# Performance work log

Measured on AMD Instinct MI355X. Metric: run time of the kernel, lower is better.

Reference implementation:

```python
import jax, jax.numpy as jnp
import numpy as np

N_EMBED = 768
N_HEAD = 12
HEAD = N_EMBED // N_HEAD
B, T = 4, 2048


def setup_inputs() -> dict:
    key = jax.random.key(0)
    ks = jax.random.split(key, 12)
    s = 0.02
    d = N_EMBED
    return {
        "x": jax.random.normal(ks[0], (B, T, d), jnp.float32),
        "ln1_g": jnp.ones((d,), jnp.float32),
        "ln1_b": jnp.zeros((d,), jnp.float32),
        "w_attn": jax.random.normal(ks[1], (d, 3 * d), jnp.float32) * s,
        "b_attn": jnp.zeros((3 * d,), jnp.float32),
        "w_aproj": jax.random.normal(ks[2], (d, d), jnp.float32) * s,
        "b_aproj": jnp.zeros((d,), jnp.float32),
        "ln2_g": jnp.ones((d,), jnp.float32),
        "ln2_b": jnp.zeros((d,), jnp.float32),
        "w_fc": jax.random.normal(ks[3], (d, 4 * d), jnp.float32) * s,
        "b_fc": jnp.zeros((4 * d,), jnp.float32),
        "w_mproj": jax.random.normal(ks[4], (4 * d, d), jnp.float32) * s,
        "b_mproj": jnp.zeros((d,), jnp.float32),
    }


def _layernorm(x, g, b, eps=1e-5):
    mu = jnp.mean(x, axis=-1, keepdims=True)
    var = jnp.var(x, axis=-1, keepdims=True)
    return (x - mu) * jax.lax.rsqrt(var + eps) * g + b


def _attn(x, w_attn, b_attn, w_aproj, b_aproj):
    Bq, Tq, C = x.shape
    qkv = x @ w_attn + b_attn  # [B,T,3C]
    q, k, v = jnp.split(qkv, 3, axis=2)
    q = q.reshape(Bq, Tq, N_HEAD, HEAD).transpose(0, 2, 1, 3)  # [B,H,T,hd]
    k = k.reshape(Bq, Tq, N_HEAD, HEAD).transpose(0, 2, 1, 3)
    v = v.reshape(Bq, Tq, N_HEAD, HEAD).transpose(0, 2, 1, 3)
    att = jnp.einsum("bhqd,bhkd->bhqk", q, k) * (1.0 / np.sqrt(HEAD))
    causal = jnp.tril(jnp.ones((Tq, Tq), bool))
    att = jnp.where(causal, att, -jnp.inf)
    att = jax.nn.softmax(att, axis=-1)
    y = jnp.einsum("bhqk,bhkd->bhqd", att, v)
    y = y.transpose(0, 2, 1, 3).reshape(Bq, Tq, C)
    return y @ w_aproj + b_aproj


def reference(x, ln1_g, ln1_b, w_attn, b_attn, w_aproj, b_aproj,
              ln2_g, ln2_b, w_fc, b_fc, w_mproj, b_mproj):
    x = x + _attn(_layernorm(x, ln1_g, ln1_b), w_attn, b_attn, w_aproj, b_aproj)
    h = _layernorm(x, ln2_g, ln2_b)
    h = jax.nn.gelu(h @ w_fc + b_fc, approximate=False)
    x = x + (h @ w_mproj + b_mproj)
    return x
```

## Files before the change

### kernel.cpp

```cpp
#include <hip/hip_runtime.h>
#include <hip/hip_bf16.h>

#define NE 768
#define NH 12
#define HD 64
#define BB 4
#define TT 2048
#define ROWS (BB*TT)

typedef __attribute__((ext_vector_type(8))) short bf16x8;
typedef __attribute__((ext_vector_type(4))) float f32x4;

__device__ __forceinline__ short f2bf(float f) {
  __hip_bfloat16 h = __float2bfloat16(f);
  union { __hip_bfloat16 h; short s; } u; u.h = h; return u.s;
}

__device__ __forceinline__ void gload16(const void* g, void* l) {
  __builtin_amdgcn_global_load_lds(
      (const __attribute__((address_space(1))) void*)g,
      (__attribute__((address_space(3))) void*)l,
      16, 0, 0);
}

__device__ __forceinline__ void xcd_remap(int id, int nbn, int& bm, int& bn) {
  int x = id & 7;
  int j = id >> 3;
  bm = x * 8 + j / nbn;
  bn = j % nbn;
}

__global__ __launch_bounds__(256) void wtrans_kernel(
    const float* __restrict__ W, short* __restrict__ Wt, int K, int N) {
  __shared__ short tile[64 * 65];
  int k0 = blockIdx.x * 64, n0 = blockIdx.y * 64;
  int t = threadIdx.x;
#pragma unroll
  for (int p = 0; p < 16; ++p) {
    int idx = p * 256 + t;
    int r = idx >> 6, c = idx & 63;
    tile[r * 65 + c] = f2bf(W[(size_t)(k0 + r) * N + n0 + c]);
  }
  __syncthreads();
#pragma unroll
  for (int p = 0; p < 16; ++p) {
    int idx = p * 256 + t;
    int rr = idx >> 6, cc = idx & 63;
    Wt[(size_t)(n0 + rr) * K + k0 + cc] = tile[cc * 65 + rr];
  }
}

__global__ __launch_bounds__(256) void vtrans_kernel(
    const short* __restrict__ qkv, short* __restrict__ vt) {
  __shared__ short tile[64 * 65];
  int bh = blockIdx.x;
  int b = bh / NH, h = bh % NH;
  int t0 = blockIdx.y * 64;
  int t = threadIdx.x;
#pragma unroll
  for (int p = 0; p < 16; ++p) {
    int idx = p * 256 + t;
    int r = idx >> 6, c = idx & 63;
    tile[r * 65 + c] =
        qkv[(size_t)(b * TT + t0 + r) * (3 * NE) + 2 * NE + h * HD + c];
  }
  __syncthreads();
#pragma unroll
  for (int p = 0; p < 16; ++p) {
    int idx = p * 256 + t;
    int rr = idx >> 6, cc = idx & 63;
    vt[(size_t)bh * HD * TT + (size_t)rr * TT + t0 + cc] = tile[cc * 65 + rr];
  }
}

__global__ __launch_bounds__(64) void ln_kernel(
    const float* __restrict__ x, const float* __restrict__ g,
    const float* __restrict__ b, short* __restrict__ out) {
  int row = blockIdx.x, l = threadIdx.x;
  const float* xr = x + (size_t)row * NE;
  float4 v[3];
  float s = 0.f, ss = 0.f;
#pragma unroll
  for (int i = 0; i < 3; ++i) {
    v[i] = *reinterpret_cast<const float4*>(xr + l * 4 + i * 256);
    s += v[i].x + v[i].y + v[i].z + v[i].w;
    ss += v[i].x * v[i].x + v[i].y * v[i].y + v[i].z * v[i].z + v[i].w * v[i].w;
  }
#pragma unroll
  for (int m = 1; m < 64; m <<= 1) {
    s += __shfl_xor(s, m);
    ss += __shfl_xor(ss, m);
  }
  float mu = s * (1.0f / NE);
  float var = ss * (1.0f / NE) - mu * mu;
  float rstd = rsqrtf(var + 1e-5f);
#pragma unroll
  for (int i = 0; i < 3; ++i) {
    float4 gv = *reinterpret_cast<const float4*>(g + l * 4 + i * 256);
    float4 bv = *reinterpret_cast<const float4*>(b + l * 4 + i * 256);
    short4 o;
    o.x = f2bf((v[i].x - mu) * rstd * gv.x + bv.x);
    o.y = f2bf((v[i].y - mu) * rstd * gv.y + bv.y);
    o.z = f2bf((v[i].z - mu) * rstd * gv.z + bv.z);
    o.w = f2bf((v[i].w - mu) * rstd * gv.w + bv.w);
    *reinterpret_cast<short4*>(out + (size_t)row * NE + l * 4 + i * 256) = o;
  }
}

template <int EPI>
__global__ __launch_bounds__(256) void gemm_kernel(
    const short* __restrict__ A, const short* __restrict__ Bt,
    const float* __restrict__ bias, const float* __restrict__ resid,
    void* __restrict__ Cout, int M, int N, int K, int nbn) {
  __shared__ short As[2][128 * 32];
  __shared__ short Bs[2][128 * 32];
  int t = threadIdx.x;
  int w = t >> 6, l = t & 63;
  int wr = w >> 1, wc = w & 1;
  int bm, bn;
  xcd_remap(blockIdx.x, nbn, bm, bn);
  int lr = l & 15, g4 = l >> 4;

  f32x4 acc[4][4];
#pragma unroll
  for (int i = 0; i < 4; ++i)
#pragma unroll
    for (int j = 0; j < 4; ++j) acc[i][j] = (f32x4){0.f, 0.f, 0.f, 0.f};

  int r0 = t >> 2;
  int cs = ((t & 3) ^ (r0 & 3)) * 8;
  const short* ga = A + (size_t)(bm * 128) * K;
  const short* gb = Bt + (size_t)(bn * 128) * K;

  gload16(ga + (size_t)r0 * K + cs, &As[0][t * 8]);
  gload16(ga + (size_t)(r0 + 64) * K + cs, &As[0][(t + 256) * 8]);
  gload16(gb + (size_t)r0 * K + cs, &Bs[0][t * 8]);
  gload16(gb + (size_t)(r0 + 64) * K + cs, &Bs[0][(t + 256) * 8]);

  int xorA = (lr & 3) << 4;
  int nk = K >> 5;
  for (int kt = 0; kt < nk; ++kt) {
    int bi = kt & 1;
    __syncthreads();
    if (kt + 1 < nk) {
      int ko = (kt + 1) * 32;
      gload16(ga + (size_t)r0 * K + ko + cs, &As[bi ^ 1][t * 8]);
      gload16(ga + (size_t)(r0 + 64) * K + ko + cs, &As[bi ^ 1][(t + 256) * 8]);
      gload16(gb + (size_t)r0 * K + ko + cs, &Bs[bi ^ 1][t * 8]);
      gload16(gb + (size_t)(r0 + 64) * K + ko + cs, &Bs[bi ^ 1][(t + 256) * 8]);
    }
    const char* Ab = (const char*)As[bi];
    const char* Bb = (const char*)Bs[bi];
    bf16x8 af[4], bfr[4];
#pragma unroll
    for (int i = 0; i < 4; ++i)
      af[i] = *reinterpret_cast<const bf16x8*>(
          Ab + (((wr * 64 + i * 16 + lr) * 64 + g4 * 16) ^ xorA));
#pragma unroll
    for (int j = 0; j < 4; ++j)
      bfr[j] = *reinterpret_cast<const bf16x8*>(
          Bb + (((wc * 64 + j * 16 + lr) * 64 + g4 * 16) ^ xorA));
#pragma unroll
    for (int i = 0; i < 4; ++i)
#pragma unroll
      for (int j = 0; j < 4; ++j)
        acc[i][j] = __builtin_amdgcn_mfma_f32_16x16x32_bf16(af[i], bfr[j], acc[i][j], 0, 0, 0);
  }

  int rbase = bm * 128 + wr * 64;
  int cbase = bn * 128 + wc * 64;
#pragma unroll
  for (int i = 0; i < 4; ++i) {
#pragma unroll
    for (int r = 0; r < 4; ++r) {
      int row = rbase + i * 16 + g4 * 4 + r;
#pragma unroll
      for (int j = 0; j < 4; ++j) {
        int col = cbase + j * 16 + lr;
        float v = acc[i][j][r] + bias[col];
        if (EPI == 0) {
          ((short*)Cout)[(size_t)row * N + col] = f2bf(v);
        } else if (EPI == 1) {
          v = 0.5f * v * (1.0f + erff(v * 0.70710678118654752f));
          ((short*)Cout)[(size_t)row * N + col] = f2bf(v);
        } else {
          ((float*)Cout)[(size_t)row * N + col] = v + resid[(size_t)row * N + col];
        }
      }
    }
  }
}

template <int EPI>
__global__ __launch_bounds__(256) void gemm64_kernel(
    const short* __restrict__ A, const short* __restrict__ Bt,
    const float* __restrict__ bias, const float* __restrict__ resid,
    void* __restrict__ Cout, int M, int N, int K, int nbn) {
  __shared__ short As[2][128 * 32];
  __shared__ short Bs[2][64 * 32];
  int t = threadIdx.x;
  int w = t >> 6, l = t & 63;
  int bm, bn;
  xcd_remap(blockIdx.x, nbn, bm, bn);
  int lr = l & 15, g4 = l >> 4;

  f32x4 acc[2][4];
#pragma unroll
  for (int i = 0; i < 2; ++i)
#pragma unroll
    for (int j = 0; j < 4; ++j) acc[i][j] = (f32x4){0.f, 0.f, 0.f, 0.f};

  int r0 = t >> 2;
  int cs = ((t & 3) ^ (r0 & 3)) * 8;
  const short* ga = A + (size_t)(bm * 128) * K;
  const short* gb = Bt + (size_t)(bn * 64) * K;

  gload16(ga + (size_t)r0 * K + cs, &As[0][t * 8]);
  gload16(ga + (size_t)(r0 + 64) * K + cs, &As[0][(t + 256) * 8]);
  gload16(gb + (size_t)r0 * K + cs, &Bs[0][t * 8]);

  int xorA = (lr & 3) << 4;
  int nk = K >> 5;
  for (int kt = 0; kt < nk; ++kt) {
    int bi = kt & 1;
    __syncthreads();
    if (kt + 1 < nk) {
      int ko = (kt + 1) * 32;
      gload16(ga + (size_t)r0 * K + ko + cs, &As[bi ^ 1][t * 8]);
      gload16(ga + (size_t)(r0 + 64) * K + ko + cs, &As[bi ^ 1][(t + 256) * 8]);
      gload16(gb + (size_t)r0 * K + ko + cs, &Bs[bi ^ 1][t * 8]);
    }
    const char* Ab = (const char*)As[bi];
    const char* Bb = (const char*)Bs[bi];
    bf16x8 af[2], bfr[4];
#pragma unroll
    for (int i = 0; i < 2; ++i)
      af[i] = *reinterpret_cast<const bf16x8*>(
          Ab + (((w * 32 + i * 16 + lr) * 64 + g4 * 16) ^ xorA));
#pragma unroll
    for (int j = 0; j < 4; ++j)
      bfr[j] = *reinterpret_cast<const bf16x8*>(
          Bb + (((j * 16 + lr) * 64 + g4 * 16) ^ xorA));
#pragma unroll
    for (int i = 0; i < 2; ++i)
#pragma unroll
      for (int j = 0; j < 4; ++j)
        acc[i][j] = __builtin_amdgcn_mfma_f32_16x16x32_bf16(af[i], bfr[j], acc[i][j], 0, 0, 0);
  }

  int rbase = bm * 128 + w * 32;
  int cbase = bn * 64;
#pragma unroll
  for (int i = 0; i < 2; ++i) {
#pragma unroll
    for (int r = 0; r < 4; ++r) {
      int row = rbase + i * 16 + g4 * 4 + r;
#pragma unroll
      for (int j = 0; j < 4; ++j) {
        int col = cbase + j * 16 + lr;
        float v = acc[i][j][r] + bias[col];
        if (EPI == 0) {
          ((short*)Cout)[(size_t)row * N + col] = f2bf(v);
        } else if (EPI == 1) {
          v = 0.5f * v * (1.0f + erff(v * 0.70710678118654752f));
          ((short*)Cout)[(size_t)row * N + col] = f2bf(v);
        } else {
          ((float*)Cout)[(size_t)row * N + col] = v + resid[(size_t)row * N + col];
        }
      }
    }
  }
}

__global__ __launch_bounds__(256, 4) void attn_kernel(
    const short* __restrict__ qkv, const short* __restrict__ vt,
    short* __restrict__ y) {
  __shared__ short Ks[2][64 * 64];
  __shared__ short Vs[2][64 * 64];
  int t = threadIdx.x, w = t >> 6, l = t & 63;
  int lr = l & 15, g = l >> 4, lkb = g * 8;
  int bh = blockIdx.x;
  int b = bh / NH, h = bh % NH;
  int qt = ((int)gridDim.y - 1) - blockIdx.y;
  int qbase = qt * 64;
  const int rstride = 3 * NE;

  const short* qrow = qkv + (size_t)(b * TT + qbase + w * 16 + lr) * rstride + h * HD + lkb;
  bf16x8 qf0 = *reinterpret_cast<const bf16x8*>(qrow);
  bf16x8 qf1 = *reinterpret_cast<const bf16x8*>(qrow + 32);

  f32x4 o[4];
#pragma unroll
  for (int j = 0; j < 4; ++j) o[j] = (f32x4){0.f, 0.f, 0.f, 0.f};
  float m_run = -3e38f, l_run = 0.f;

  int ci0 = t, ci1 = t + 256;
  int row0 = ci0 >> 3, c0 = ((ci0 & 7) ^ (row0 & 7)) * 8;
  int row1 = ci1 >> 3, c1 = ((ci1 & 7) ^ (row1 & 7)) * 8;

  const short* kbase = qkv + (size_t)(b * TT) * rstride + NE + h * HD;
  const short* vtb = vt + (size_t)bh * HD * TT;

  gload16(kbase + (size_t)row0 * rstride + c0, &Ks[0][ci0 * 8]);
  gload16(kbase + (size_t)row1 * rstride + c1, &Ks[0][ci1 * 8]);
  gload16(vtb + (size_t)row0 * TT + c0, &Vs[0][ci0 * 8]);
  gload16(vtb + (size_t)row1 * TT + c1, &Vs[0][ci1 * 8]);

  int qmin = qbase + w * 16;
  int srcA = ((g & 1) * 2) * 16 + lr;
  int srcB = srcA + 16;
  bool ghi = (g >= 2);

  int nkv = qt + 1;
  for (int kt = 0; kt < nkv; ++kt) {
    int bi = kt & 1;
    int kvbase = kt * 64;
    bool pre = (kt + 1 < nkv);
    __syncthreads();

    if (pre) {
      int nb = kvbase + 64;
      gload16(kbase + (size_t)(nb + row0) * rstride + c0, &Ks[bi ^ 1][ci0 * 8]);
      gload16(kbase + (size_t)(nb + row1) * rstride + c1, &Ks[bi ^ 1][ci1 * 8]);
      gload16(vtb + (size_t)row0 * TT + nb + c0, &Vs[bi ^ 1][ci0 * 8]);
      gload16(vtb + (size_t)row1 * TT + nb + c1, &Vs[bi ^ 1][ci1 * 8]);
    }

    f32x4 s[4];
#pragma unroll
    for (int nt = 0; nt < 4; ++nt) {
      int row = nt * 16 + lr;
      bf16x8 kf0 = *reinterpret_cast<const bf16x8*>(
          (char*)Ks[bi] + ((row * 128 + lkb * 2) ^ ((lr & 7) << 4)));
      bf16x8 kf1 = *reinterpret_cast<const bf16x8*>(
          (char*)Ks[bi] + ((row * 128 + 64 + lkb * 2) ^ ((lr & 7) << 4)));
      f32x4 st = (f32x4){0.f, 0.f, 0.f, 0.f};
      st = __builtin_amdgcn_mfma_f32_16x16x32_bf16(kf0, qf0, st, 0, 0, 0);
      st = __builtin_amdgcn_mfma_f32_16x16x32_bf16(kf1, qf1, st, 0, 0, 0);
      s[nt] = st;
    }

    if (kvbase + 63 > qmin) {
      int qabs = qmin + lr;
#pragma unroll
      for (int nt = 0; nt < 4; ++nt)
#pragma unroll
        for (int r = 0; r < 4; ++r) {
          int kp = kvbase + nt * 16 + g * 4 + r;
          s[nt][r] = (kp <= qabs) ? s[nt][r] * 0.125f : -3e38f;
        }
    } else {
#pragma unroll
      for (int nt = 0; nt < 4; ++nt)
#pragma unroll
        for (int r = 0; r < 4; ++r)
          s[nt][r] *= 0.125f;
    }

    float mx = s[0][0];
#pragma unroll
    for (int nt = 0; nt < 4; ++nt)
#pragma unroll
      for (int r = 0; r < 4; ++r) mx = fmaxf(mx, s[nt][r]);
    mx = fmaxf(mx, __shfl_xor(mx, 16));
    mx = fmaxf(mx, __shfl_xor(mx, 32));
    if (__any(mx > m_run + 8.f)) {
      float mn = fmaxf(m_run, mx);
      float al = __expf(m_run - mn);
      m_run = mn;
      l_run *= al;
      float al0 = __shfl(al, g * 4 + 0);
      float al1 = __shfl(al, g * 4 + 1);
      float al2 = __shfl(al, g * 4 + 2);
      float al3 = __shfl(al, g * 4 + 3);
#pragma unroll
      for (int j = 0; j < 4; ++j) {
        o[j][0] *= al0; o[j][1] *= al1; o[j][2] *= al2; o[j][3] *= al3;
      }
    }
    float rs = 0.f;
#pragma unroll
    for (int nt = 0; nt < 4; ++nt)
#pragma unroll
      for (int r = 0; r < 4; ++r) {
        float p = __expf(s[nt][r] - m_run);
        s[nt][r] = p;
        rs += p;
      }
    rs += __shfl_xor(rs, 16);
    rs += __shfl_xor(rs, 32);
    l_run += rs;

    unsigned int pw[4][2];
#pragma unroll
    for (int nt = 0; nt < 4; ++nt)
#pragma unroll
      for (int pr = 0; pr < 2; ++pr)
        pw[nt][pr] = (unsigned int)(unsigned short)f2bf(s[nt][2 * pr]) |
                     ((unsigned int)(unsigned short)f2bf(s[nt][2 * pr + 1]) << 16);

#pragma unroll
    for (int c = 0; c < 2; ++c) {
      unsigned int a00 = __shfl(pw[c * 2 + 0][0], srcA);
      unsigned int a01 = __shfl(pw[c * 2 + 0][1], srcA);
      unsigned int a02 = __shfl(pw[c * 2 + 0][0], srcB);
      unsigned int a03 = __shfl(pw[c * 2 + 0][1], srcB);
      unsigned int a10 = __shfl(pw[c * 2 + 1][0], srcA);
      unsigned int a11 = __shfl(pw[c * 2 + 1][1], srcA);
      unsigned int a12 = __shfl(pw[c * 2 + 1][0], srcB);
      unsigned int a13 = __shfl(pw[c * 2 + 1][1], srcB);
      unsigned int u0 = ghi ? a10 : a00;
      unsigned int u1 = ghi ? a11 : a01;
      unsigned int u2 = ghi ? a12 : a02;
      unsigned int u3 = ghi ? a13 : a03;
      bf16x8 pa;
      pa[0] = (short)(u0 & 0xffffu); pa[1] = (short)(u0 >> 16);
      pa[2] = (short)(u1 & 0xffffu); pa[3] = (short)(u1 >> 16);
      pa[4] = (short)(u2 & 0xffffu); pa[5] = (short)(u2 >> 16);
      pa[6] = (short)(u3 & 0xffffu); pa[7] = (short)(u3 >> 16);
#pragma unroll
      for (int j = 0; j < 4; ++j) {
        int vrow = j * 16 + lr;
        bf16x8 vf = *reinterpret_cast<const bf16x8*>(
            (char*)Vs[bi] + ((vrow * 128 + c * 64 + lkb * 2) ^ ((lr & 7) << 4)));
        o[j] = __builtin_amdgcn_mfma_f32_16x16x32_bf16(pa, vf, o[j], 0, 0, 0);
      }
    }
  }

  float inv = 1.0f / l_run;
  float i0 = __shfl(inv, g * 4 + 0);
  float i1 = __shfl(inv, g * 4 + 1);
  float i2 = __shfl(inv, g * 4 + 2);
  float i3 = __shfl(inv, g * 4 + 3);
#pragma unroll
  for (int r = 0; r < 4; ++r) {
    float ir = (r == 0) ? i0 : (r == 1) ? i1 : (r == 2) ? i2 : i3;
    size_t row = (size_t)(b * TT + qbase + w * 16 + g * 4 + r);
#pragma unroll
    for (int j = 0; j < 4; ++j)
      y[row * NE + h * HD + j * 16 + lr] = f2bf(o[j][r] * ir);
  }
}

extern "C" void kernel_launch(void* const* d_in, const int* in_sizes, int n_in,
                              void* d_out, int out_size, void* d_ws, size_t ws_size,
                              hipStream_t stream) {
  (void)in_sizes; (void)n_in; (void)out_size; (void)ws_size;
  const float* x       = (const float*)d_in[0];
  const float* ln1_g   = (const float*)d_in[1];
  const float* ln1_b   = (const float*)d_in[2];
  const float* w_attn  = (const float*)d_in[3];
  const float* b_attn  = (const float*)d_in[4];
  const float* w_aproj = (const float*)d_in[5];
  const float* b_aproj = (const float*)d_in[6];
  const float* ln2_g   = (const float*)d_in[7];
  const float* ln2_b   = (const float*)d_in[8];
  const float* w_fc    = (const float*)d_in[9];
  const float* b_fc    = (const float*)d_in[10];
  const float* w_mproj = (const float*)d_in[11];
  const float* b_mproj = (const float*)d_in[12];

  char* ws = (char*)d_ws;
  size_t off = 0;
  auto alloc = [&](size_t bytes) {
    char* p = ws + off;
    off += (bytes + 255) & ~(size_t)255;
    return p;
  };
  short* wt_attn  = (short*)alloc((size_t)2304 * 768 * 2);
  short* wt_aproj = (short*)alloc((size_t)768 * 768 * 2);
  short* wt_fc    = (short*)alloc((size_t)3072 * 768 * 2);
  short* wt_mproj = (short*)alloc((size_t)768 * 3072 * 2);
  short* lnb  = (short*)alloc((size_t)ROWS * 768 * 2);
  short* qkvb = (short*)alloc((size_t)ROWS * 3072 * 2);
  short* yb   = (short*)alloc((size_t)ROWS * 768 * 2);
  float* x2   = (float*)alloc((size_t)ROWS * 768 * 4);
  short* vtg = lnb;

  wtrans_kernel<<<dim3(768 / 64, 2304 / 64), 256, 0, stream>>>(w_attn, wt_attn, 768, 2304);
  wtrans_kernel<<<dim3(768 / 64, 768 / 64), 256, 0, stream>>>(w_aproj, wt_aproj, 768, 768);
  wtrans_kernel<<<dim3(768 / 64, 3072 / 64), 256, 0, stream>>>(w_fc, wt_fc, 768, 3072);
  wtrans_kernel<<<dim3(3072 / 64, 768 / 64), 256, 0, stream>>>(w_mproj, wt_mproj, 3072, 768);

  ln_kernel<<<ROWS, 64, 0, stream>>>(x, ln1_g, ln1_b, lnb);
  gemm_kernel<0><<<64 * 18, 256, 0, stream>>>(
      lnb, wt_attn, b_attn, nullptr, qkvb, ROWS, 2304, 768, 18);
  vtrans_kernel<<<dim3(BB * NH, TT / 64), 256, 0, stream>>>(qkvb, vtg);
  attn_kernel<<<dim3(BB * NH, TT / 64), 256, 0, stream>>>(qkvb, vtg, yb);
  gemm64_kernel<2><<<64 * 12, 256, 0, stream>>>(
      yb, wt_aproj, b_aproj, x, x2, ROWS, 768, 768, 12);
  ln_kernel<<<ROWS, 64, 0, stream>>>(x2, ln2_g, ln2_b, lnb);
  gemm_kernel<1><<<64 * 24, 256, 0, stream>>>(
      lnb, wt_fc, b_fc, nullptr, qkvb, ROWS, 3072, 768, 24);
  gemm64_kernel<2><<<64 * 12, 256, 0, stream>>>(
      qkvb, wt_mproj, b_mproj, x2, (float*)d_out, ROWS, 768, 3072, 12);
}
```

Measured before the change: 306.9 us.

## Deepen GEMM LDS prefetch pipelines with explicit vmcnt waits

```diff
diff --git a/kernel.cpp b/kernel.cpp
--- a/kernel.cpp
+++ b/kernel.cpp
@@ -10,6 +10,14 @@
 
 typedef __attribute__((ext_vector_type(8))) short bf16x8;
 typedef __attribute__((ext_vector_type(4))) float f32x4;
+
+#define WAITV(N) asm volatile("s_waitcnt vmcnt(" #N ")" ::: "memory")
+#define BARSYNC()                                   \
+  do {                                              \
+    __builtin_amdgcn_sched_barrier(0);              \
+    __builtin_amdgcn_s_barrier();                   \
+    __builtin_amdgcn_sched_barrier(0);              \
+  } while (0)
 
 __device__ __forceinline__ short f2bf(float f) {
   __hip_bfloat16 h = __float2bfloat16(f);
@@ -112,8 +120,8 @@
     const short* __restrict__ A, const short* __restrict__ Bt,
     const float* __restrict__ bias, const float* __restrict__ resid,
     void* __restrict__ Cout, int M, int N, int K, int nbn) {
-  __shared__ short As[2][128 * 32];
-  __shared__ short Bs[2][128 * 32];
+  __shared__ short As[3][128 * 32];
+  __shared__ short Bs[3][128 * 32];
   int t = threadIdx.x;
   int w = t >> 6, l = t & 63;
   int wr = w >> 1, wc = w & 1;
@@ -132,25 +140,31 @@
   const short* ga = A + (size_t)(bm * 128) * K;
   const short* gb = Bt + (size_t)(bn * 128) * K;
 
-  gload16(ga + (size_t)r0 * K + cs, &As[0][t * 8]);
-  gload16(ga + (size_t)(r0 + 64) * K + cs, &As[0][(t + 256) * 8]);
-  gload16(gb + (size_t)r0 * K + cs, &Bs[0][t * 8]);
-  gload16(gb + (size_t)(r0 + 64) * K + cs, &Bs[0][(t + 256) * 8]);
+#pragma unroll
+  for (int p = 0; p < 2; ++p) {
+    int ko = p * 32;
+    gload16(ga + (size_t)r0 * K + ko + cs, &As[p][t * 8]);
+    gload16(ga + (size_t)(r0 + 64) * K + ko + cs, &As[p][(t + 256) * 8]);
+    gload16(gb + (size_t)r0 * K + ko + cs, &Bs[p][t * 8]);
+    gload16(gb + (size_t)(r0 + 64) * K + ko + cs, &Bs[p][(t + 256) * 8]);
+  }
 
   int xorA = (lr & 3) << 4;
   int nk = K >> 5;
+  int cur = 0, prv = 2;
   for (int kt = 0; kt < nk; ++kt) {
-    int bi = kt & 1;
-    __syncthreads();
-    if (kt + 1 < nk) {
-      int ko = (kt + 1) * 32;
-      gload16(ga + (size_t)r0 * K + ko + cs, &As[bi ^ 1][t * 8]);
-      gload16(ga + (size_t)(r0 + 64) * K + ko + cs, &As[bi ^ 1][(t + 256) * 8]);
-      gload16(gb + (size_t)r0 * K + ko + cs, &Bs[bi ^ 1][t * 8]);
-      gload16(gb + (size_t)(r0 + 64) * K + ko + cs, &Bs[bi ^ 1][(t + 256) * 8]);
-    }
-    const char* Ab = (const char*)As[bi];
-    const char* Bb = (const char*)Bs[bi];
+    if (kt < nk - 1) WAITV(4); else WAITV(0);
+    BARSYNC();
+    if (kt + 2 < nk) {
+      int ko = (kt + 2) * 32;
+      gload16(ga + (size_t)r0 * K + ko + cs, &As[prv][t * 8]);
+      gload16(ga + (size_t)(r0 + 64) * K + ko + cs, &As[prv][(t + 256) * 8]);
+      gload16(gb + (size_t)r0 * K + ko + cs, &Bs[prv][t * 8]);
+      gload16(gb + (size_t)(r0 + 64) * K + ko + cs, &Bs[prv][(t + 256) * 8]);
+    }
+    __builtin_amdgcn_sched_barrier(0);
+    const char* Ab = (const char*)As[cur];
+    const char* Bb = (const char*)Bs[cur];
     bf16x8 af[4], bfr[4];
 #pragma unroll
     for (int i = 0; i < 4; ++i)
@@ -165,6 +179,8 @@
 #pragma unroll
       for (int j = 0; j < 4; ++j)
         acc[i][j] = __builtin_amdgcn_mfma_f32_16x16x32_bf16(af[i], bfr[j], acc[i][j], 0, 0, 0);
+    prv = cur;
+    cur = (cur == 2) ? 0 : cur + 1;
   }
 
   int rbase = bm * 128 + wr * 64;
@@ -196,8 +212,8 @@
     const short* __restrict__ A, const short* __restrict__ Bt,
     const float* __restrict__ bias, const float* __restrict__ resid,
     void* __restrict__ Cout, int M, int N, int K, int nbn) {
-  __shared__ short As[2][128 * 32];
-  __shared__ short Bs[2][64 * 32];
+  __shared__ short As[4][128 * 32];
+  __shared__ short Bs[4][64 * 32];
   int t = threadIdx.x;
   int w = t >> 6, l = t & 63;
   int bm, bn;
@@ -215,21 +231,31 @@
   const short* ga = A + (size_t)(bm * 128) * K;
   const short* gb = Bt + (size_t)(bn * 64) * K;
 
-  gload16(ga + (size_t)r0 * K + cs, &As[0][t * 8]);
-  gload16(ga + (size_t)(r0 + 64) * K + cs, &As[0][(t + 256) * 8]);
-  gload16(gb + (size_t)r0 * K + cs, &Bs[0][t * 8]);
+#pragma unroll
+  for (int p = 0; p < 3; ++p) {
+    int ko = p * 32;
+    gload16(ga + (size_t)r0 * K + ko + cs, &As[p][t * 8]);
+    gload16(ga + (size_t)(r0 + 64) * K + ko + cs, &As[p][(t + 256) * 8]);
+    gload16(gb + (size_t)r0 * K + ko + cs, &Bs[p][t * 8]);
+  }
 
   int xorA = (lr & 3) << 4;
   int nk = K >> 5;
   for (int kt = 0; kt < nk; ++kt) {
-    int bi = kt & 1;
-    __syncthreads();
-    if (kt + 1 < nk) {
-      int ko = (kt + 1) * 32;
-      gload16(ga + (size_t)r0 * K + ko + cs, &As[bi ^ 1][t * 8]);
-      gload16(ga + (size_t)(r0 + 64) * K + ko + cs, &As[bi ^ 1][(t + 256) * 8]);
-      gload16(gb + (size_t)r0 * K + ko + cs, &Bs[bi ^ 1][t * 8]);
-    }
+    int bi = kt & 3;
+    int rem = nk - 1 - kt;
+    if (rem >= 2) WAITV(6);
+    else if (rem == 1) WAITV(3);
+    else WAITV(0);
+    BARSYNC();
+    if (kt + 3 < nk) {
+      int ko = (kt + 3) * 32;
+      int nb = (kt + 3) & 3;
+      gload16(ga + (size_t)r0 * K + ko + cs, &As[nb][t * 8]);
+      gload16(ga + (size_t)(r0 + 64) * K + ko + cs, &As[nb][(t + 256) * 8]);
+      gload16(gb + (size_t)r0 * K + ko + cs, &Bs[nb][t * 8]);
+    }
+    __builtin_amdgcn_sched_barrier(0);
     const char* Ab = (const char*)As[bi];
     const char* Bb = (const char*)Bs[bi];
     bf16x8 af[2], bfr[4];
```

Result: no change. 303.9 us (-1.0%).
